# Kernel optimization log

Measured on AMD Instinct MI355X. Metric: run time of the kernel, lower is better.

Reference implementation:

```python
import jax, jax.numpy as jnp
import numpy as np

D_MODEL = 1024
NUM_HEADS = 16
HEAD_DIM = D_MODEL // NUM_HEADS
MASK_FUTURE = False
NEG_INF = -1.0e9


def setup_inputs() -> dict:
    key = jax.random.key(0)
    ks = jax.random.split(key, 8)
    B, L = 2, 2048
    q = jax.random.normal(ks[0], (B, L, D_MODEL), dtype=jnp.float32)
    k = jax.random.normal(ks[1], (B, L, D_MODEL), dtype=jnp.float32)
    v = jax.random.normal(ks[2], (B, L, D_MODEL), dtype=jnp.float32)
    attention_mask = jnp.ones((B, L), dtype=jnp.int32)
    s = 1.0 / np.sqrt(D_MODEL)
    Wq = jax.random.normal(ks[3], (D_MODEL, D_MODEL), dtype=jnp.float32) * s
    Wk = jax.random.normal(ks[4], (D_MODEL, D_MODEL), dtype=jnp.float32) * s
    Wv = jax.random.normal(ks[5], (D_MODEL, D_MODEL), dtype=jnp.float32) * s
    Wo = jax.random.normal(ks[6], (D_MODEL, D_MODEL), dtype=jnp.float32) * s
    return {"q": q, "k": k, "v": v, "attention_mask": attention_mask,
            "Wq": Wq, "Wk": Wk, "Wv": Wv, "Wo": Wo}


def _split_heads(x):
    B, L, _ = x.shape
    return x.reshape(B, L, NUM_HEADS, HEAD_DIM).transpose(0, 2, 1, 3)  # [B,H,L,Hd]


def reference(q, k, v, attention_mask, Wq, Wk, Wv, Wo):
    B, Lq, _ = q.shape
    Lk = k.shape[1]
    Q = _split_heads(q @ Wq.T)
    K = _split_heads(k @ Wk.T)
    V = _split_heads(v @ Wv.T)
    scale = HEAD_DIM ** 0.5  # per-head D in original Attention
    scores = jnp.einsum('bhqd,bhkd->bhqk', Q, K) / scale
    mask = (attention_mask == 0)[:, None, None, :]  # [B,1,1,Lk]
    scores = jnp.where(mask, NEG_INF, scores)
    if MASK_FUTURE:
        fut = jnp.triu(jnp.ones((Lq, Lk), dtype=bool), k=1)
        scores = jnp.where(fut[None, None], NEG_INF, scores)
    attn = jax.nn.softmax(scores, axis=-1)
    out = jnp.einsum('bhqk,bhkd->bhqd', attn, V)
    out = out.transpose(0, 2, 1, 3).reshape(B, Lq, D_MODEL)
    return out @ Wo.T
```

## Files before the change

### kernel.cpp

```cpp
#include <hip/hip_runtime.h>


#define D_MODEL 1024
#define NH 16
#define HD 64
#define BATCH 2
#define SEQ 2048
#define MROWS (BATCH*SEQ)

typedef unsigned short u16;
typedef __bf16 bf16x8 __attribute__((ext_vector_type(8)));
typedef float f32x4 __attribute__((ext_vector_type(4)));
typedef float f32x16 __attribute__((ext_vector_type(16)));

__device__ __forceinline__ u16 f2bf(float f){
    __bf16 h = (__bf16)f;
    return __builtin_bit_cast(u16, h);
}
__device__ __forceinline__ float fast_exp2(float x){ return __builtin_amdgcn_exp2f(x); }

__device__ __forceinline__ void stage16(const void* g, void* l){
#if __has_builtin(__builtin_amdgcn_global_load_lds)
    __builtin_amdgcn_global_load_lds(
        (__attribute__((address_space(1))) void*)(unsigned long long)(g),
        (__attribute__((address_space(3))) void*)(unsigned int)(unsigned long long)(l),
        16, 0, 0);
#else
    *(uint4*)l = *(const uint4*)g;
#endif
}

__device__ __forceinline__ int detect_f32_block(const u16* q, int tid){
    __shared__ int flag;
    if (tid < 64){
        unsigned e = (q[2*tid]>>7)&0xFFu;
        bool hit = (e>=115u)&&(e<=132u);
        unsigned long long m = __ballot(hit);
        if (tid==0) flag = (__popcll(m) < 32) ? 1 : 0;
    }
    __syncthreads();
    return flag;
}

__global__ __launch_bounds__(256)
void convert_all(const u16* __restrict__ q, const u16* __restrict__ k,
                 const u16* __restrict__ v, const u16* __restrict__ Wq,
                 const u16* __restrict__ Wk, const u16* __restrict__ Wv,
                 const u16* __restrict__ Wo, u16* __restrict__ dst)
{
    int isf32 = detect_f32_block(q, threadIdx.x);
    int bid = blockIdx.x;
    const u16* src; int lb;
    if      (bid < 4096)  { src=q;  lb=bid; }
    else if (bid < 8192)  { src=k;  lb=bid-4096; }
    else if (bid < 12288) { src=v;  lb=bid-8192; }
    else if (bid < 13312) { src=Wq; lb=bid-12288; }
    else if (bid < 14336) { src=Wk; lb=bid-13312; }
    else if (bid < 15360) { src=Wv; lb=bid-14336; }
    else                  { src=Wo; lb=bid-15360; }
    size_t so = (size_t)lb*1024 + threadIdx.x*4;
    size_t dofs = (size_t)bid*1024 + threadIdx.x*4;
    if (isf32){
        float4 x = *(const float4*)((const float*)src + so);
        ushort4 o; o.x=f2bf(x.x); o.y=f2bf(x.y); o.z=f2bf(x.z); o.w=f2bf(x.w);
        *(ushort4*)(dst+dofs) = o;
    } else {
        *(ushort4*)(dst+dofs) = *(const ushort4*)(src+so);
    }
}

__global__ __launch_bounds__(256)
void gemm_qkv(const u16* __restrict__ qb, const u16* __restrict__ kb,
              const u16* __restrict__ vb, const u16* __restrict__ Wqb,
              const u16* __restrict__ Wkb, const u16* __restrict__ Wvb,
              u16* __restrict__ Qh, u16* __restrict__ Kh, u16* __restrict__ Vt)
{
    const int K = 1024;
    __shared__ __align__(16) u16 lA[128*32];
    __shared__ __align__(16) u16 lB[128*32];
    const int z = blockIdx.z;
    const u16* A  = (z==0)? qb  : (z==1)? kb  : vb;
    const u16* Bt = (z==0)? Wqb : (z==1)? Wkb : Wvb;

    const int tid  = threadIdx.x;
    const int wid  = tid>>6, lane = tid&63;
    const int quad = lane>>4, l16 = lane&15;
    const int wm = (wid>>1)*64, wn = (wid&1)*64;
    const int row0 = blockIdx.y*128, col0 = blockIdx.x*128;

    f32x4 acc[4][4];
    #pragma unroll
    for (int i=0;i<4;i++)
        #pragma unroll
        for (int j=0;j<4;j++) acc[i][j] = (f32x4){0.f,0.f,0.f,0.f};

    for (int k0=0; k0<K; k0+=32){
        #pragma unroll
        for (int s=0;s<2;s++){
            int c = tid + s*256;
            int r = c>>2, cc = (c&3)*8;
            stage16(&A [(size_t)(row0+r)*K + k0 + cc], &lA[c*8]);
            stage16(&Bt[(size_t)(col0+r)*K + k0 + cc], &lB[c*8]);
        }
        __syncthreads();
        bf16x8 af[4], bfr[4];
        #pragma unroll
        for (int mi=0;mi<4;mi++) af[mi]  = *(const bf16x8*)&lA[(wm+mi*16+l16)*32 + quad*8];
        #pragma unroll
        for (int ni=0;ni<4;ni++) bfr[ni] = *(const bf16x8*)&lB[(wn+ni*16+l16)*32 + quad*8];
        #pragma unroll
        for (int mi=0;mi<4;mi++)
            #pragma unroll
            for (int ni=0;ni<4;ni++)
                acc[mi][ni] = __builtin_amdgcn_mfma_f32_16x16x32_bf16(af[mi], bfr[ni], acc[mi][ni], 0,0,0);
        __syncthreads();
    }

    const float qsc = (z==0) ? 0.18033688011112042f : 1.0f;
    u16* Csh = (z==0)? Qh : Kh;
    #pragma unroll
    for (int mi=0;mi<4;mi++){
        #pragma unroll
        for (int ni=0;ni<4;ni++){
            int col = col0 + wn + ni*16 + l16;
            #pragma unroll
            for (int r=0;r<4;r++){
                int row = row0 + wm + mi*16 + quad*4 + r;
                u16 o = f2bf(acc[mi][ni][r]*qsc);
                int b = row>>11, i = row&2047, h = col>>6, d = col&63;
                if (z<2) Csh[((((size_t)(b*NH+h))*SEQ + i)<<6) + d] = o;
                else     Vt[((size_t)((b*NH+h)*HD + d))*SEQ + i] = o;
            }
        }
    }
}

__global__ __launch_bounds__(256)
void gemm_out(const u16* __restrict__ A, const u16* __restrict__ Bt,
              void* __restrict__ Cv, const u16* __restrict__ qref)
{
    const int K = 1024, N = 1024;
    int outf32 = detect_f32_block(qref, threadIdx.x);
    __shared__ __align__(16) u16 lA[64*32];
    __shared__ __align__(16) u16 lB[128*32];
    const int tid  = threadIdx.x;
    const int wid  = tid>>6, lane = tid&63;
    const int quad = lane>>4, l16 = lane&15;
    const int wm = (wid>>1)*32, wn = (wid&1)*64;
    const int row0 = blockIdx.y*64, col0 = blockIdx.x*128;

    f32x4 acc[2][4];
    #pragma unroll
    for (int i=0;i<2;i++)
        #pragma unroll
        for (int j=0;j<4;j++) acc[i][j] = (f32x4){0.f,0.f,0.f,0.f};

    for (int k0=0; k0<K; k0+=32){
        {
            int r = tid>>2, cc = (tid&3)*8;
            stage16(&A[(size_t)(row0+r)*K + k0 + cc], &lA[tid*8]);
        }
        #pragma unroll
        for (int s=0;s<2;s++){
            int c = tid + s*256;
            int r = c>>2, cc = (c&3)*8;
            stage16(&Bt[(size_t)(col0+r)*K + k0 + cc], &lB[c*8]);
        }
        __syncthreads();
        bf16x8 af[2], bfr[4];
        #pragma unroll
        for (int mi=0;mi<2;mi++) af[mi]  = *(const bf16x8*)&lA[(wm+mi*16+l16)*32 + quad*8];
        #pragma unroll
        for (int ni=0;ni<4;ni++) bfr[ni] = *(const bf16x8*)&lB[(wn+ni*16+l16)*32 + quad*8];
        #pragma unroll
        for (int mi=0;mi<2;mi++)
            #pragma unroll
            for (int ni=0;ni<4;ni++)
                acc[mi][ni] = __builtin_amdgcn_mfma_f32_16x16x32_bf16(af[mi], bfr[ni], acc[mi][ni], 0,0,0);
        __syncthreads();
    }

    #pragma unroll
    for (int mi=0;mi<2;mi++){
        #pragma unroll
        for (int ni=0;ni<4;ni++){
            int col = col0 + wn + ni*16 + l16;
            #pragma unroll
            for (int r=0;r<4;r++){
                int row = row0 + wm + mi*16 + quad*4 + r;
                float f = acc[mi][ni][r];
                if (outf32) ((float*)Cv)[(size_t)row*N + col] = f;
                else        ((u16*)Cv)[(size_t)row*N + col] = f2bf(f);
            }
        }
    }
}

#define KVT 4096
#define VROW 68
#define VVT (64*VROW)
#define SW(row, c8) ((row)*64 + ((((c8) ^ ((row)&7)))*8))

__global__ __launch_bounds__(512, 4)
void attn3(const u16* __restrict__ Qh, const u16* __restrict__ Kh,
           const u16* __restrict__ Vt, const int* __restrict__ mask,
           u16* __restrict__ ctx)
{
    __shared__ __align__(16) u16 smem[4*KVT + 4*VVT];
    __shared__ unsigned mb[64];

    const int id = blockIdx.x;
    const int bh = (id&7)*4 + (id>>7);
    const int qb = (id>>3)&15;
    const int b = bh>>4, h = bh&15;
    const int i0 = qb*128;
    const int tid = threadIdx.x;
    const int wv = tid>>6, lane = tid&63;
    const int l31 = lane&31, hi = lane>>5;
    const int hf = tid>>8;
    const int lt = tid&255;
    const int wq = wv&3;

    u16* lkh = smem + (hf*2)*KVT;
    u16* lvh = smem + 4*KVT + (hf*2)*VVT;

    const u16* Kp  = Kh + (size_t)bh*SEQ*HD + (size_t)hf*1024*HD;
    const u16* Vtp = Vt + (size_t)bh*HD*SEQ + hf*1024;
    const int* mp  = mask + b*SEQ;

    if (tid < 64){
        unsigned w = 0;
        #pragma unroll 8
        for (int i=0;i<32;i++) w |= (mp[tid*32+i] ? 1u:0u) << i;
        mb[tid] = w;
    }
    #pragma unroll
    for (int s=0;s<2;s++){
        int c = lt + s*256;
        int r = c>>3, c8 = c&7;
        *(uint4*)&lkh[SW(r,c8)] = *(const uint4*)&Kp[(size_t)r*HD + c8*8];
        uint4 x = *(const uint4*)&Vtp[(size_t)r*SEQ + c8*8];
        uint2 xl; xl.x = x.x; xl.y = x.y;
        uint2 xh; xh.x = x.z; xh.y = x.w;
        *(uint2*)&lvh[r*VROW + c8*8]     = xl;
        *(uint2*)&lvh[r*VROW + c8*8 + 4] = xh;
    }

    const u16* Qrow = Qh + ((size_t)bh*SEQ + i0 + wq*32 + l31)*HD;
    bf16x8 aq[4];
    #pragma unroll
    for (int kk=0;kk<4;kk++) aq[kk] = *(const bf16x8*)&Qrow[kk*16 + hi*8];

    bf16x8 bones;
    #pragma unroll
    for (int j=0;j<8;j++) ((u16*)&bones)[j] = 0x3F80;

    f32x16 Oacc[2], Lacc;
    #pragma unroll
    for (int r=0;r<16;r++){ Oacc[0][r]=0.f; Oacc[1][r]=0.f; Lacc[r]=0.f; }

    for (int t=0; t<16; t++){
        u16* lkc = lkh + (t&1)*KVT;
        u16* lvc = lvh + (t&1)*VVT;
        u16* lkn = lkh + ((t&1)^1)*KVT;
        u16* lvn = lvh + ((t&1)^1)*VVT;

        __syncthreads();

        uint4 gk[2], gv[2];
        if (t < 15){
            #pragma unroll
            for (int s=0;s<2;s++){
                int c = lt + s*256;
                int r = c>>3, c8 = c&7;
                gk[s] = *(const uint4*)&Kp[(size_t)(t*64+64+r)*HD + c8*8];
                gv[s] = *(const uint4*)&Vtp[(size_t)r*SEQ + t*64+64 + c8*8];
            }
        }

        __builtin_amdgcn_s_setprio(1);
        #pragma unroll
        for (int jt=0; jt<2; ++jt){
            f32x16 sfr;
            #pragma unroll
            for (int r=0;r<16;r++) sfr[r]=0.f;
            #pragma unroll
            for (int kk=0;kk<4;kk++){
                bf16x8 ak = *(const bf16x8*)&lkc[SW(jt*32+l31, 2*kk+hi)];
                sfr = __builtin_amdgcn_mfma_f32_32x32x16_bf16(ak, aq[kk], sfr, 0,0,0);
            }

            unsigned mw = mb[(hf*16+t)*2 + jt];
            if ((unsigned)__builtin_amdgcn_readfirstlane((int)mw) != 0xFFFFFFFFu){
                unsigned ms = mw >> (hi*4);
                #pragma unroll
                for (int r=0;r<16;r++){
                    int kb = (r&3)+8*(r>>2);
                    if (!((ms>>kb)&1u)) sfr[r] = -1.0e9f;
                }
            }

            unsigned cc[8];
            #pragma unroll
            for (int d=0; d<8; ++d){
                float p0 = fast_exp2(sfr[2*d]);
                float p1 = fast_exp2(sfr[2*d+1]);
                cc[d] = (unsigned)f2bf(p0) | ((unsigned)f2bf(p1)<<16);
            }
            bf16x8 pa0, pa1;
            ((unsigned*)&pa0)[0]=cc[0]; ((unsigned*)&pa0)[1]=cc[1];
            ((unsigned*)&pa0)[2]=cc[2]; ((unsigned*)&pa0)[3]=cc[3];
            ((unsigned*)&pa1)[0]=cc[4]; ((unsigned*)&pa1)[1]=cc[5];
            ((unsigned*)&pa1)[2]=cc[6]; ((unsigned*)&pa1)[3]=cc[7];

            Lacc = __builtin_amdgcn_mfma_f32_32x32x16_bf16(pa0, bones, Lacc, 0,0,0);
            Lacc = __builtin_amdgcn_mfma_f32_32x32x16_bf16(pa1, bones, Lacc, 0,0,0);

            #pragma unroll
            for (int dn=0; dn<2; ++dn){
                int vrb = (dn*32 + l31)*VROW + jt*32 + 4*hi;
                uint2 a0 = *(const uint2*)&lvc[vrb];
                uint2 a1 = *(const uint2*)&lvc[vrb + 8];
                uint2 b0 = *(const uint2*)&lvc[vrb + 16];
                uint2 b1 = *(const uint2*)&lvc[vrb + 24];
                union { uint4 u; bf16x8 v; } bv0, bv1;
                bv0.u.x=a0.x; bv0.u.y=a0.y; bv0.u.z=a1.x; bv0.u.w=a1.y;
                bv1.u.x=b0.x; bv1.u.y=b0.y; bv1.u.z=b1.x; bv1.u.w=b1.y;
                Oacc[dn] = __builtin_amdgcn_mfma_f32_32x32x16_bf16(pa0, bv0.v, Oacc[dn], 0,0,0);
                Oacc[dn] = __builtin_amdgcn_mfma_f32_32x32x16_bf16(pa1, bv1.v, Oacc[dn], 0,0,0);
            }
        }
        __builtin_amdgcn_s_setprio(0);

        if (t < 15){
            #pragma unroll
            for (int s=0;s<2;s++){
                int c = lt + s*256;
                int r = c>>3, c8 = c&7;
                *(uint4*)&lkn[SW(r,c8)] = gk[s];
                uint2 xl; xl.x = gv[s].x; xl.y = gv[s].y;
                uint2 xh; xh.x = gv[s].z; xh.y = gv[s].w;
                *(uint2*)&lvn[r*VROW + c8*8]     = xl;
                *(uint2*)&lvn[r*VROW + c8*8 + 4] = xh;
            }
        }
    }

    __syncthreads();
    float* mrg = (float*)smem;
    if (hf == 1){
        float* p = mrg + (size_t)(wq*64 + lane)*49;
        #pragma unroll
        for (int dn=0; dn<2; ++dn)
            #pragma unroll
            for (int r=0;r<16;r++) p[dn*16+r] = Oacc[dn][r];
        #pragma unroll
        for (int r=0;r<16;r++) p[32+r] = Lacc[r];
    }
    __syncthreads();
    if (hf == 0){
        const float* p = mrg + (size_t)(wq*64 + lane)*49;
        #pragma unroll
        for (int dn=0; dn<2; ++dn)
            #pragma unroll
            for (int r=0;r<16;r++) Oacc[dn][r] += p[dn*16+r];
        float rc[16];
        #pragma unroll
        for (int r=0;r<16;r++) rc[r] = 1.0f / (Lacc[r] + p[32+r]);
        #pragma unroll
        for (int dn=0; dn<2; ++dn){
            int col = h*HD + dn*32 + l31;
            #pragma unroll
            for (int r=0;r<16;r++){
                int row = i0 + wq*32 + (r&3) + 8*(r>>2) + 4*hi;
                ctx[((size_t)(b*SEQ+row))*D_MODEL + col] = f2bf(Oacc[dn][r] * rc[r]);
            }
        }
    }
}

extern "C" void kernel_launch(void* const* d_in, const int* in_sizes, int n_in,
                              void* d_out, int out_size, void* d_ws, size_t ws_size,
                              hipStream_t stream)
{
    (void)in_sizes; (void)n_in; (void)out_size; (void)ws_size;
    const u16* q    = (const u16*)d_in[0];
    const u16* k    = (const u16*)d_in[1];
    const u16* v    = (const u16*)d_in[2];
    const int* mask = (const int*)d_in[3];
    const u16* Wq   = (const u16*)d_in[4];
    const u16* Wk   = (const u16*)d_in[5];
    const u16* Wv   = (const u16*)d_in[6];
    const u16* Wo   = (const u16*)d_in[7];

    const size_t TEN = (size_t)MROWS * D_MODEL;
    const size_t WEL = (size_t)D_MODEL * D_MODEL;
    u16* qb  = (u16*)d_ws;
    u16* kb  = qb + TEN;
    u16* vb  = kb + TEN;
    u16* Wqb = vb + TEN;
    u16* Wkb = Wqb + WEL;
    u16* Wvb = Wkb + WEL;
    u16* Wob = Wvb + WEL;
    u16* Qh  = Wob + WEL;
    u16* Kh  = Qh + TEN;
    u16* Vtr = Kh + TEN;
    u16* ctx = Vtr + TEN;

    dim3 bb(256);
    convert_all<<<dim3(16384), bb, 0, stream>>>(q,k,v,Wq,Wk,Wv,Wo, qb);
    gemm_qkv<<<dim3(8,32,3), bb, 0, stream>>>(qb,kb,vb, Wqb,Wkb,Wvb, Qh,Kh,Vtr);
    attn3<<<dim3(512), dim3(512), 0, stream>>>(Qh, Kh, Vtr, mask, ctx);
    gemm_out<<<dim3(8,64), bb, 0, stream>>>(ctx, Wob, d_out, q);
}
```

Baseline: 227.2 us.

## Fuse activation fp32-to-bf16 conversion into QKV GEMM and remap blocks per XCD

Activation conversion no longer runs as a separate pass. gemm_qkv now reads the fp32 q/k/v directly, converts them to bf16 in registers and writes them to LDS, and only the weights still go through a standalone conversion kernel. This removes writing and re-reading about 24 MB of bf16 activation copies. Both GEMMs also remap block IDs so that blocks sharing A rows land on the same XCD, which should improve L2 reuse. In exchange, the A-tile staging becomes a synchronous register path instead of direct global-to-LDS loads, and each tile re-reads A in fp32 (twice the bytes), relying on cache reuse across the column blocks.

```diff
diff --git a/kernel.cpp b/kernel.cpp
--- a/kernel.cpp
+++ b/kernel.cpp
@@ -43,21 +43,14 @@
 }
 
 __global__ __launch_bounds__(256)
-void convert_all(const u16* __restrict__ q, const u16* __restrict__ k,
-                 const u16* __restrict__ v, const u16* __restrict__ Wq,
-                 const u16* __restrict__ Wk, const u16* __restrict__ Wv,
-                 const u16* __restrict__ Wo, u16* __restrict__ dst)
+void convert_w(const u16* __restrict__ q, const u16* __restrict__ Wq,
+               const u16* __restrict__ Wk, const u16* __restrict__ Wv,
+               const u16* __restrict__ Wo, u16* __restrict__ dst)
 {
     int isf32 = detect_f32_block(q, threadIdx.x);
     int bid = blockIdx.x;
-    const u16* src; int lb;
-    if      (bid < 4096)  { src=q;  lb=bid; }
-    else if (bid < 8192)  { src=k;  lb=bid-4096; }
-    else if (bid < 12288) { src=v;  lb=bid-8192; }
-    else if (bid < 13312) { src=Wq; lb=bid-12288; }
-    else if (bid < 14336) { src=Wk; lb=bid-13312; }
-    else if (bid < 15360) { src=Wv; lb=bid-14336; }
-    else                  { src=Wo; lb=bid-15360; }
+    int w = bid>>10, lb = bid&1023;
+    const u16* src = (w==0)? Wq : (w==1)? Wk : (w==2)? Wv : Wo;
     size_t so = (size_t)lb*1024 + threadIdx.x*4;
     size_t dofs = (size_t)bid*1024 + threadIdx.x*4;
     if (isf32){
@@ -70,23 +63,30 @@
 }
 
 __global__ __launch_bounds__(256)
-void gemm_qkv(const u16* __restrict__ qb, const u16* __restrict__ kb,
-              const u16* __restrict__ vb, const u16* __restrict__ Wqb,
+void gemm_qkv(const u16* __restrict__ qr, const u16* __restrict__ kr,
+              const u16* __restrict__ vr, const u16* __restrict__ Wqb,
               const u16* __restrict__ Wkb, const u16* __restrict__ Wvb,
               u16* __restrict__ Qh, u16* __restrict__ Kh, u16* __restrict__ Vt)
 {
     const int K = 1024;
+    int isf32 = detect_f32_block(qr, threadIdx.x);
     __shared__ __align__(16) u16 lA[128*32];
     __shared__ __align__(16) u16 lB[128*32];
-    const int z = blockIdx.z;
-    const u16* A  = (z==0)? qb  : (z==1)? kb  : vb;
+
+    const int lid = blockIdx.x + 8*(blockIdx.y + 32*blockIdx.z);
+    const int xcd = lid & 7, loc = lid >> 3;
+    const int xb = loc & 7, p = loc >> 3;
+    const int yz = xcd*12 + p;
+    const int z = yz >> 5, yb = yz & 31;
+
+    const u16* A  = (z==0)? qr  : (z==1)? kr  : vr;
     const u16* Bt = (z==0)? Wqb : (z==1)? Wkb : Wvb;
 
     const int tid  = threadIdx.x;
     const int wid  = tid>>6, lane = tid&63;
     const int quad = lane>>4, l16 = lane&15;
     const int wm = (wid>>1)*64, wn = (wid&1)*64;
-    const int row0 = blockIdx.y*128, col0 = blockIdx.x*128;
+    const int row0 = yb*128, col0 = xb*128;
 
     f32x4 acc[4][4];
     #pragma unroll
@@ -99,8 +99,30 @@
         for (int s=0;s<2;s++){
             int c = tid + s*256;
             int r = c>>2, cc = (c&3)*8;
-            stage16(&A [(size_t)(row0+r)*K + k0 + cc], &lA[c*8]);
             stage16(&Bt[(size_t)(col0+r)*K + k0 + cc], &lB[c*8]);
+        }
+        if (isf32){
+            const float* Af = (const float*)A;
+            #pragma unroll
+            for (int s=0;s<2;s++){
+                int c = tid + s*256;
+                int r = c>>2, cc = (c&3)*8;
+                const float* src = &Af[(size_t)(row0+r)*K + k0 + cc];
+                float4 x0 = *(const float4*)src;
+                float4 x1 = *(const float4*)(src+4);
+                ushort4 o0, o1;
+                o0.x=f2bf(x0.x); o0.y=f2bf(x0.y); o0.z=f2bf(x0.z); o0.w=f2bf(x0.w);
+                o1.x=f2bf(x1.x); o1.y=f2bf(x1.y); o1.z=f2bf(x1.z); o1.w=f2bf(x1.w);
+                *(ushort4*)&lA[c*8]   = o0;
+                *(ushort4*)&lA[c*8+4] = o1;
+            }
+        } else {
+            #pragma unroll
+            for (int s=0;s<2;s++){
+                int c = tid + s*256;
+                int r = c>>2, cc = (c&3)*8;
+                *(uint4*)&lA[c*8] = *(const uint4*)&A[(size_t)(row0+r)*K + k0 + cc];
+            }
         }
         __syncthreads();
         bf16x8 af[4], bfr[4];
@@ -147,7 +169,11 @@
     const int wid  = tid>>6, lane = tid&63;
     const int quad = lane>>4, l16 = lane&15;
     const int wm = (wid>>1)*32, wn = (wid&1)*64;
-    const int row0 = blockIdx.y*64, col0 = blockIdx.x*128;
+
+    const int lid = blockIdx.x + 8*blockIdx.y;
+    const int xcd = lid & 7, loc = lid >> 3;
+    const int xb = loc & 7, yb = xcd*8 + (loc>>3);
+    const int row0 = yb*64, col0 = xb*128;
 
     f32x4 acc[2][4];
     #pragma unroll
@@ -395,10 +421,7 @@
 
     const size_t TEN = (size_t)MROWS * D_MODEL;
     const size_t WEL = (size_t)D_MODEL * D_MODEL;
-    u16* qb  = (u16*)d_ws;
-    u16* kb  = qb + TEN;
-    u16* vb  = kb + TEN;
-    u16* Wqb = vb + TEN;
+    u16* Wqb = (u16*)d_ws;
     u16* Wkb = Wqb + WEL;
     u16* Wvb = Wkb + WEL;
     u16* Wob = Wvb + WEL;
@@ -408,8 +431,8 @@
     u16* ctx = Vtr + TEN;
 
     dim3 bb(256);
-    convert_all<<<dim3(16384), bb, 0, stream>>>(q,k,v,Wq,Wk,Wv,Wo, qb);
-    gemm_qkv<<<dim3(8,32,3), bb, 0, stream>>>(qb,kb,vb, Wqb,Wkb,Wvb, Qh,Kh,Vtr);
+    convert_w<<<dim3(4096), bb, 0, stream>>>(q, Wq,Wk,Wv,Wo, Wqb);
+    gemm_qkv<<<dim3(8,32,3), bb, 0, stream>>>(q,k,v, Wqb,Wkb,Wvb, Qh,Kh,Vtr);
     attn3<<<dim3(512), dim3(512), 0, stream>>>(Qh, Kh, Vtr, mask, ctx);
     gemm_out<<<dim3(8,64), bb, 0, stream>>>(ctx, Wob, d_out, q);
 }
```

Result: no change. 226.6 us (-0.3%).

## Deepen GEMM K-tile to 64 with XOR-swizzled LDS and XCD-aware block remap

Applied to the files above, without the earlier changes.

Both projection GEMMs now stage 64-wide K slices per iteration instead of 32, which halves the number of barrier pairs. The LDS layout is XOR-swizzled by row so the fragment reads avoid bank conflicts. Block indices are remapped so that blocks landing on the same XCD share rows or columns of A, which is meant to improve L2 reuse. The trade-offs are double the LDS footprint per block, which may reduce occupancy, and extra index arithmetic.

```diff
diff --git a/kernel.cpp b/kernel.cpp
--- a/kernel.cpp
+++ b/kernel.cpp
@@ -76,9 +76,15 @@
               u16* __restrict__ Qh, u16* __restrict__ Kh, u16* __restrict__ Vt)
 {
     const int K = 1024;
-    __shared__ __align__(16) u16 lA[128*32];
-    __shared__ __align__(16) u16 lB[128*32];
-    const int z = blockIdx.z;
+    __shared__ __align__(16) u16 lA[128*64];
+    __shared__ __align__(16) u16 lB[128*64];
+
+    const int lid = blockIdx.x + 8*(blockIdx.y + 32*blockIdx.z);
+    const int xcd = lid & 7, loc = lid >> 3;
+    const int xb = loc & 7, p = loc >> 3;
+    const int yz = xcd*12 + p;
+    const int z = yz >> 5, yb = yz & 31;
+
     const u16* A  = (z==0)? qb  : (z==1)? kb  : vb;
     const u16* Bt = (z==0)? Wqb : (z==1)? Wkb : Wvb;
 
@@ -86,7 +92,7 @@
     const int wid  = tid>>6, lane = tid&63;
     const int quad = lane>>4, l16 = lane&15;
     const int wm = (wid>>1)*64, wn = (wid&1)*64;
-    const int row0 = blockIdx.y*128, col0 = blockIdx.x*128;
+    const int row0 = yb*128, col0 = xb*128;
 
     f32x4 acc[4][4];
     #pragma unroll
@@ -94,25 +100,35 @@
         #pragma unroll
         for (int j=0;j<4;j++) acc[i][j] = (f32x4){0.f,0.f,0.f,0.f};
 
-    for (int k0=0; k0<K; k0+=32){
-        #pragma unroll
-        for (int s=0;s<2;s++){
+    for (int k0=0; k0<K; k0+=64){
+        #pragma unroll
+        for (int s=0;s<4;s++){
             int c = tid + s*256;
-            int r = c>>2, cc = (c&3)*8;
-            stage16(&A [(size_t)(row0+r)*K + k0 + cc], &lA[c*8]);
-            stage16(&Bt[(size_t)(col0+r)*K + k0 + cc], &lB[c*8]);
+            int row = c>>3, cr = c&7;
+            int gc = cr ^ (row&7);
+            stage16(&A [(size_t)(row0+row)*K + k0 + gc*8], &lA[c*8]);
+            stage16(&Bt[(size_t)(col0+row)*K + k0 + gc*8], &lB[c*8]);
         }
         __syncthreads();
-        bf16x8 af[4], bfr[4];
-        #pragma unroll
-        for (int mi=0;mi<4;mi++) af[mi]  = *(const bf16x8*)&lA[(wm+mi*16+l16)*32 + quad*8];
-        #pragma unroll
-        for (int ni=0;ni<4;ni++) bfr[ni] = *(const bf16x8*)&lB[(wn+ni*16+l16)*32 + quad*8];
-        #pragma unroll
-        for (int mi=0;mi<4;mi++)
-            #pragma unroll
-            for (int ni=0;ni<4;ni++)
-                acc[mi][ni] = __builtin_amdgcn_mfma_f32_16x16x32_bf16(af[mi], bfr[ni], acc[mi][ni], 0,0,0);
+        #pragma unroll
+        for (int kk=0;kk<2;kk++){
+            bf16x8 af[4], bfr[4];
+            #pragma unroll
+            for (int mi=0;mi<4;mi++){
+                int r = wm + mi*16 + l16;
+                af[mi] = *(const bf16x8*)&lA[r*64 + ((kk*4+quad) ^ (r&7))*8];
+            }
+            #pragma unroll
+            for (int ni=0;ni<4;ni++){
+                int r = wn + ni*16 + l16;
+                bfr[ni] = *(const bf16x8*)&lB[r*64 + ((kk*4+quad) ^ (r&7))*8];
+            }
+            #pragma unroll
+            for (int mi=0;mi<4;mi++)
+                #pragma unroll
+                for (int ni=0;ni<4;ni++)
+                    acc[mi][ni] = __builtin_amdgcn_mfma_f32_16x16x32_bf16(af[mi], bfr[ni], acc[mi][ni], 0,0,0);
+        }
         __syncthreads();
     }
 
@@ -141,13 +157,17 @@
 {
     const int K = 1024, N = 1024;
     int outf32 = detect_f32_block(qref, threadIdx.x);
-    __shared__ __align__(16) u16 lA[64*32];
-    __shared__ __align__(16) u16 lB[128*32];
+    __shared__ __align__(16) u16 lA[64*64];
+    __shared__ __align__(16) u16 lB[128*64];
     const int tid  = threadIdx.x;
     const int wid  = tid>>6, lane = tid&63;
     const int quad = lane>>4, l16 = lane&15;
     const int wm = (wid>>1)*32, wn = (wid&1)*64;
-    const int row0 = blockIdx.y*64, col0 = blockIdx.x*128;
+
+    const int lid = blockIdx.x + 8*blockIdx.y;
+    const int xcd = lid & 7, loc = lid >> 3;
+    const int xb = loc & 7, yb = xcd*8 + (loc>>3);
+    const int row0 = yb*64, col0 = xb*128;
 
     f32x4 acc[2][4];
     #pragma unroll
@@ -155,28 +175,41 @@
         #pragma unroll
         for (int j=0;j<4;j++) acc[i][j] = (f32x4){0.f,0.f,0.f,0.f};
 
-    for (int k0=0; k0<K; k0+=32){
-        {
-            int r = tid>>2, cc = (tid&3)*8;
-            stage16(&A[(size_t)(row0+r)*K + k0 + cc], &lA[tid*8]);
-        }
+    for (int k0=0; k0<K; k0+=64){
         #pragma unroll
         for (int s=0;s<2;s++){
             int c = tid + s*256;
-            int r = c>>2, cc = (c&3)*8;
-            stage16(&Bt[(size_t)(col0+r)*K + k0 + cc], &lB[c*8]);
+            int row = c>>3, cr = c&7;
+            int gc = cr ^ (row&7);
+            stage16(&A[(size_t)(row0+row)*K + k0 + gc*8], &lA[c*8]);
+        }
+        #pragma unroll
+        for (int s=0;s<4;s++){
+            int c = tid + s*256;
+            int row = c>>3, cr = c&7;
+            int gc = cr ^ (row&7);
+            stage16(&Bt[(size_t)(col0+row)*K + k0 + gc*8], &lB[c*8]);
         }
         __syncthreads();
-        bf16x8 af[2], bfr[4];
-        #pragma unroll
-        for (int mi=0;mi<2;mi++) af[mi]  = *(const bf16x8*)&lA[(wm+mi*16+l16)*32 + quad*8];
-        #pragma unroll
-        for (int ni=0;ni<4;ni++) bfr[ni] = *(const bf16x8*)&lB[(wn+ni*16+l16)*32 + quad*8];
-        #pragma unroll
-        for (int mi=0;mi<2;mi++)
-            #pragma unroll
-            for (int ni=0;ni<4;ni++)
-                acc[mi][ni] = __builtin_amdgcn_mfma_f32_16x16x32_bf16(af[mi], bfr[ni], acc[mi][ni], 0,0,0);
+        #pragma unroll
+        for (int kk=0;kk<2;kk++){
+            bf16x8 af[2], bfr[4];
+            #pragma unroll
+            for (int mi=0;mi<2;mi++){
+                int r = wm + mi*16 + l16;
+                af[mi] = *(const bf16x8*)&lA[r*64 + ((kk*4+quad) ^ (r&7))*8];
+            }
+            #pragma unroll
+            for (int ni=0;ni<4;ni++){
+                int r = wn + ni*16 + l16;
+                bfr[ni] = *(const bf16x8*)&lB[r*64 + ((kk*4+quad) ^ (r&7))*8];
+            }
+            #pragma unroll
+            for (int mi=0;mi<2;mi++)
+                #pragma unroll
+                for (int ni=0;ni<4;ni++)
+                    acc[mi][ni] = __builtin_amdgcn_mfma_f32_16x16x32_bf16(af[mi], bfr[ni], acc[mi][ni], 0,0,0);
+        }
         __syncthreads();
     }
 
```

Result: slower. 233.1 us (+2.6%).
